# Kernel optimization log

Measured on AMD Instinct MI355X. Metric: run time of the kernel, lower is better.

Reference implementation:

```python
import jax, jax.numpy as jnp
import numpy as np

HIDDEN = 512
HEADS = 8
HEAD_DIM = HIDDEN // HEADS


def setup_inputs() -> dict:
    key = jax.random.key(0)
    ks = jax.random.split(key, 12)
    B, S = 2, 2048
    s = 1.0 / np.sqrt(HIDDEN)
    inp = {
        "query": jax.random.normal(ks[0], (B, S, HIDDEN), dtype=jnp.float32),
        "key": jax.random.normal(ks[1], (B, S, HIDDEN), dtype=jnp.float32),
        "value": jax.random.normal(ks[2], (B, S, HIDDEN), dtype=jnp.float32),
        "Wq": jax.random.uniform(ks[3], (HIDDEN, HIDDEN), jnp.float32, -s, s),
        "bq": jnp.zeros((HIDDEN,), jnp.float32),
        "Wk": jax.random.uniform(ks[4], (HIDDEN, HIDDEN), jnp.float32, -s, s),
        "bk": jnp.zeros((HIDDEN,), jnp.float32),
        "Wv": jax.random.uniform(ks[5], (HIDDEN, HIDDEN), jnp.float32, -s, s),
        "bv": jnp.zeros((HIDDEN,), jnp.float32),
        "Wo": jax.random.uniform(ks[6], (HIDDEN, HIDDEN), jnp.float32, -s, s),
        "bo": jnp.zeros((HIDDEN,), jnp.float32),
    }
    return inp


def reference(query, key, value, Wq, bq, Wk, bk, Wv, bv, Wo, bo):
    B, S, _ = query.shape
    scale = jnp.sqrt(jnp.asarray(HEAD_DIM, dtype=query.dtype))
    # Linear projections (torch Linear: x @ W.T + b)
    Q = (query @ Wq.T + bq).reshape(B, S, HEADS, HEAD_DIM).transpose(0, 2, 1, 3)
    K = (key @ Wk.T + bk).reshape(B, S, HEADS, HEAD_DIM).transpose(0, 2, 1, 3)
    V = (value @ Wv.T + bv).reshape(B, S, HEADS, HEAD_DIM).transpose(0, 2, 1, 3)
    # Scores: [B, H, S, S]
    energy = jnp.einsum("bhqd,bhkd->bhqk", Q, K) / scale
    attn = jax.nn.softmax(energy, axis=-1)
    # Dropout is identity in eval mode.
    x = jnp.einsum("bhqk,bhkd->bhqd", attn, V)
    x = x.transpose(0, 2, 1, 3).reshape(B, S, HIDDEN)
    return x @ Wo.T + bo
```

## Files before the change

### kernel.cpp

```cpp
#include <hip/hip_runtime.h>

typedef __bf16 bf16x8 __attribute__((ext_vector_type(8)));
typedef float f32x4 __attribute__((ext_vector_type(4)));
typedef unsigned int uint4v __attribute__((ext_vector_type(4)));

__device__ __forceinline__ unsigned short f2bf(float f) {
  union { float f; unsigned int u; } v; v.f = f;
  unsigned int u = v.u;
  u += 0x7FFFu + ((u >> 16) & 1u);
  return (unsigned short)(u >> 16);
}

__device__ __forceinline__ unsigned int pack2bf(float a, float b) {
  return (unsigned int)f2bf(a) | ((unsigned int)f2bf(b) << 16);
}

__global__ __launch_bounds__(256) void convert_kernel(
    const float* q, const float* k, const float* v,
    const float* wq, const float* wk, const float* wv, const float* wo,
    unsigned short* qc, unsigned short* kc, unsigned short* vc,
    unsigned short* wqc, unsigned short* wkc, unsigned short* wvc,
    unsigned short* woc, float qscale)
{
  const float* src; unsigned short* dst; int n; float sc = 1.f;
  switch (blockIdx.y) {
    case 0: src = q;  dst = qc;  n = 1 << 21; break;
    case 1: src = k;  dst = kc;  n = 1 << 21; break;
    case 2: src = v;  dst = vc;  n = 1 << 21; break;
    case 3: src = wq; dst = wqc; n = 1 << 18; sc = qscale; break;
    case 4: src = wk; dst = wkc; n = 1 << 18; break;
    case 5: src = wv; dst = wvc; n = 1 << 18; break;
    default: src = wo; dst = woc; n = 1 << 18; break;
  }
  int idx = (blockIdx.x * 256 + threadIdx.x) * 8;
  if (idx >= n) return;
  f32x4 a = *(const f32x4*)(src + idx);
  f32x4 b = *(const f32x4*)(src + idx + 4);
  uint4v p;
  p.x = pack2bf(a.x * sc, a.y * sc);
  p.y = pack2bf(a.z * sc, a.w * sc);
  p.z = pack2bf(b.x * sc, b.y * sc);
  p.w = pack2bf(b.z * sc, b.w * sc);
  *(uint4v*)(dst + idx) = p;
}

template<int OUT>
__device__ __forceinline__ void gemm_core(
    const unsigned short* __restrict__ A, const unsigned short* __restrict__ W,
    const float* __restrict__ bias, void* __restrict__ Cp,
    float bscale, int mbase, int nbase)
{
  __shared__ union {
    struct { unsigned short As[64][40]; unsigned short Bs[128][40]; } t;
    unsigned short Cs[128][72];
  } u;

  const int tid  = threadIdx.x;
  const int wave = tid >> 6, lane = tid & 63;
  const int lrow = lane & 15, lgrp = lane >> 4;

  const int ar = tid >> 2, ac = (tid & 3) * 8;
  const unsigned short* Ag  = A + (size_t)(mbase + ar) * 512 + ac;
  const unsigned short* Bg0 = W + (size_t)(nbase + ar) * 512 + ac;
  const unsigned short* Bg1 = W + (size_t)(nbase + ar + 64) * 512 + ac;

  f32x4 acc[4][2];
#pragma unroll
  for (int i = 0; i < 4; i++)
#pragma unroll
    for (int j = 0; j < 2; j++) acc[i][j] = (f32x4){0.f, 0.f, 0.f, 0.f};

  uint4v pA  = *(const uint4v*)Ag;
  uint4v pB0 = *(const uint4v*)Bg0;
  uint4v pB1 = *(const uint4v*)Bg1;

  for (int kt = 0; kt < 512; kt += 32) {
    __syncthreads();
    *(uint4v*)&u.t.As[ar][ac]      = pA;
    *(uint4v*)&u.t.Bs[ar][ac]      = pB0;
    *(uint4v*)&u.t.Bs[ar + 64][ac] = pB1;
    __syncthreads();
    if (kt + 32 < 512) {
      pA  = *(const uint4v*)(Ag  + kt + 32);
      pB0 = *(const uint4v*)(Bg0 + kt + 32);
      pB1 = *(const uint4v*)(Bg1 + kt + 32);
    }
    bf16x8 a[4], b[2];
#pragma unroll
    for (int mi = 0; mi < 4; mi++)
      a[mi] = *(const bf16x8*)&u.t.As[mi * 16 + lrow][lgrp * 8];
#pragma unroll
    for (int ni = 0; ni < 2; ni++)
      b[ni] = *(const bf16x8*)&u.t.Bs[wave * 32 + ni * 16 + lrow][lgrp * 8];
#pragma unroll
    for (int mi = 0; mi < 4; mi++)
#pragma unroll
      for (int ni = 0; ni < 2; ni++)
        acc[mi][ni] = __builtin_amdgcn_mfma_f32_16x16x32_bf16(
            a[mi], b[ni], acc[mi][ni], 0, 0, 0);
  }

  if constexpr (OUT == 2) {
    __syncthreads();
#pragma unroll
    for (int ni = 0; ni < 2; ni++) {
      int col_l = wave * 32 + ni * 16 + lrow;
      float bv = bias[nbase + col_l];
#pragma unroll
      for (int mi = 0; mi < 4; mi++) {
        int row_l = mi * 16 + lgrp * 4;
#pragma unroll
        for (int r = 0; r < 4; r++)
          u.Cs[col_l][row_l + r] = f2bf(acc[mi][ni][r] + bv);
      }
    }
    __syncthreads();
    const int bb = mbase >> 11, s_base = mbase & 2047;
    unsigned short* Vt = (unsigned short*)Cp;
#pragma unroll
    for (int ks = 0; ks < 4; ks++) {
      int seg = tid + ks * 256;
      int c = seg >> 3, r0 = (seg & 7) * 8;
      uint4v val = *(const uint4v*)&u.Cs[c][r0];
      int n = nbase + c, hh = n >> 6, d = n & 63;
      *(uint4v*)(Vt + ((size_t)(bb * 8 + hh) * 64 + d) * 2048 + s_base + r0) = val;
    }
  } else {
#pragma unroll
    for (int ni = 0; ni < 2; ni++) {
      int col = nbase + wave * 32 + ni * 16 + lrow;
      float bv = bias[col] * bscale;
#pragma unroll
      for (int mi = 0; mi < 4; mi++) {
        int row0 = mbase + mi * 16 + lgrp * 4;
#pragma unroll
        for (int r = 0; r < 4; r++) {
          float val = acc[mi][ni][r] + bv;
          if constexpr (OUT == 0)
            ((unsigned short*)Cp)[(size_t)(row0 + r) * 512 + col] = f2bf(val);
          else
            ((float*)Cp)[(size_t)(row0 + r) * 512 + col] = val;
        }
      }
    }
  }
}

__global__ __launch_bounds__(256) void qkv_gemm(
    const unsigned short* qc, const unsigned short* kc, const unsigned short* vc,
    const unsigned short* wqc, const unsigned short* wkc, const unsigned short* wvc,
    const float* bq, const float* bk, const float* bv,
    unsigned short* Qb, unsigned short* Kb, unsigned short* Vt, float qscale)
{
  const int z = blockIdx.z;
  const int mb = blockIdx.y * 64, nb = blockIdx.x * 128;
  if (z == 2)      gemm_core<2>(vc, wvc, bv, Vt, 1.f, mb, nb);
  else if (z == 0) gemm_core<0>(qc, wqc, bq, Qb, qscale, mb, nb);
  else             gemm_core<0>(kc, wkc, bk, Kb, 1.f, mb, nb);
}

__global__ __launch_bounds__(256) void out_gemm(
    const unsigned short* ctx, const unsigned short* woc,
    const float* bo, float* out)
{
  gemm_core<1>(ctx, woc, bo, out, 1.f, blockIdx.y * 64, blockIdx.x * 128);
}

__global__ __launch_bounds__(256) void attn_kernel(
    const unsigned short* Qb, const unsigned short* Kb,
    const unsigned short* Vt, unsigned short* ctx)
{
  __shared__ unsigned short Ks[128][74];
  __shared__ unsigned short Vs[64][132];
  __shared__ unsigned short Ps[64][132];

  const int tid  = threadIdx.x;
  const int wave = tid >> 6, lane = tid & 63;
  const int lrow = lane & 15, lgrp = lane >> 4;
  const int bh = blockIdx.y, b = bh >> 3, h = bh & 7;
  const int qbase = blockIdx.x * 64;

  const unsigned short* Qg  = Qb + (size_t)(b * 2048 + qbase) * 512 + h * 64;
  const unsigned short* Kg  = Kb + (size_t)(b * 2048) * 512 + h * 64;
  const unsigned short* Vtg = Vt + (size_t)bh * 64 * 2048;

#pragma unroll
  for (int i = 0; i < 2; i++) {
    int seg = tid + i * 256;
    int row = seg >> 3, c0 = (seg & 7) * 8;
    *(uint4v*)&Ps[row][c0] = *(const uint4v*)(Qg + (size_t)row * 512 + c0);
  }
  __syncthreads();
  bf16x8 qf0 = *(const bf16x8*)&Ps[wave * 16 + lrow][lgrp * 8];
  bf16x8 qf1 = *(const bf16x8*)&Ps[wave * 16 + lrow][32 + lgrp * 8];

  const int kr_ = tid >> 3, kc_ = (tid & 7) * 8;
  const int vd_ = tid >> 4, vc_ = (tid & 15) * 8;
  const int slot0 = ((kr_ & 7) << 4) | (kr_ >> 3);

  float lst[4] = {0.f, 0.f, 0.f, 0.f};
  f32x4 oacc[4];
#pragma unroll
  for (int d = 0; d < 4; d++) oacc[d] = (f32x4){0.f, 0.f, 0.f, 0.f};

  uint4v kr[4], vr[4];
#pragma unroll
  for (int i = 0; i < 4; i++) {
    kr[i] = *(const uint4v*)(Kg + (size_t)(kr_ + 32 * i) * 512 + kc_);
    vr[i] = *(const uint4v*)(Vtg + (size_t)(vd_ + 16 * i) * 2048 + vc_);
  }

  for (int it = 0; it < 16; ++it) {
    __syncthreads();
#pragma unroll
    for (int i = 0; i < 4; i++) {
      *(uint4v*)&Ks[slot0 + 4 * i][kc_] = kr[i];
      *(uint4v*)&Vs[vd_ + 16 * i][vc_]  = vr[i];
    }
    __syncthreads();
    if (it < 15) {
      const int key0 = (it + 1) * 128;
#pragma unroll
      for (int i = 0; i < 4; i++) {
        kr[i] = *(const uint4v*)(Kg + (size_t)(key0 + kr_ + 32 * i) * 512 + kc_);
        vr[i] = *(const uint4v*)(Vtg + (size_t)(vd_ + 16 * i) * 2048 + key0 + vc_);
      }
    }

    f32x4 sacc[8];
#pragma unroll
    for (int ni = 0; ni < 8; ni++) sacc[ni] = (f32x4){0.f, 0.f, 0.f, 0.f};
#pragma unroll
    for (int ni = 0; ni < 8; ni++) {
      bf16x8 k0 = *(const bf16x8*)&Ks[ni * 16 + lrow][lgrp * 8];
      bf16x8 k1 = *(const bf16x8*)&Ks[ni * 16 + lrow][32 + lgrp * 8];
      sacc[ni] = __builtin_amdgcn_mfma_f32_16x16x32_bf16(qf0, k0, sacc[ni], 0, 0, 0);
      sacc[ni] = __builtin_amdgcn_mfma_f32_16x16x32_bf16(qf1, k1, sacc[ni], 0, 0, 0);
    }

#pragma unroll
    for (int ni = 0; ni < 8; ni++)
#pragma unroll
      for (int r = 0; r < 4; r++) {
        float p = exp2f(sacc[ni][r]);
        sacc[ni][r] = p;
        lst[r] += p;
      }

#pragma unroll
    for (int r = 0; r < 4; r++) {
      uint4v pk;
      pk.x = pack2bf(sacc[0][r], sacc[1][r]);
      pk.y = pack2bf(sacc[2][r], sacc[3][r]);
      pk.z = pack2bf(sacc[4][r], sacc[5][r]);
      pk.w = pack2bf(sacc[6][r], sacc[7][r]);
      *(uint4v*)&Ps[wave * 16 + lgrp * 4 + r][lrow * 8] = pk;
    }

#pragma unroll
    for (int ks = 0; ks < 4; ks++) {
      bf16x8 pa = *(const bf16x8*)&Ps[wave * 16 + lrow][ks * 32 + lgrp * 8];
#pragma unroll
      for (int dt = 0; dt < 4; dt++) {
        bf16x8 vb = *(const bf16x8*)&Vs[dt * 16 + lrow][ks * 32 + lgrp * 8];
        oacc[dt] = __builtin_amdgcn_mfma_f32_16x16x32_bf16(pa, vb, oacc[dt], 0, 0, 0);
      }
    }
  }

#pragma unroll
  for (int m = 1; m < 16; m <<= 1)
#pragma unroll
    for (int r = 0; r < 4; r++) lst[r] += __shfl_xor(lst[r], m, 64);

  float inv[4];
#pragma unroll
  for (int r = 0; r < 4; r++) inv[r] = 1.0f / lst[r];
  unsigned short* Cg = ctx + (size_t)(b * 2048 + qbase) * 512 + h * 64;
#pragma unroll
  for (int dt = 0; dt < 4; dt++)
#pragma unroll
    for (int r = 0; r < 4; r++) {
      int row = wave * 16 + lgrp * 4 + r;
      int col = dt * 16 + lrow;
      Cg[(size_t)row * 512 + col] = f2bf(oacc[dt][r] * inv[r]);
    }
}

extern "C" void kernel_launch(void* const* d_in, const int* in_sizes, int n_in,
                              void* d_out, int out_size, void* d_ws, size_t ws_size,
                              hipStream_t stream)
{
  const float* q  = (const float*)d_in[0];
  const float* k  = (const float*)d_in[1];
  const float* v  = (const float*)d_in[2];
  const float* Wq = (const float*)d_in[3];
  const float* bq = (const float*)d_in[4];
  const float* Wk = (const float*)d_in[5];
  const float* bk = (const float*)d_in[6];
  const float* Wv = (const float*)d_in[7];
  const float* bv = (const float*)d_in[8];
  const float* Wo = (const float*)d_in[9];
  const float* bo = (const float*)d_in[10];
  float* out = (float*)d_out;

  unsigned short* qc  = (unsigned short*)d_ws;
  unsigned short* kc  = qc  + (size_t)1 * (1 << 21);
  unsigned short* vc  = qc  + (size_t)2 * (1 << 21);
  unsigned short* wqc = qc  + (size_t)3 * (1 << 21);
  unsigned short* wkc = wqc + (1 << 18);
  unsigned short* wvc = wkc + (1 << 18);
  unsigned short* woc = wvc + (1 << 18);
  unsigned short* Qb  = woc + (1 << 18);
  unsigned short* Kb  = Qb  + (1 << 22);
  unsigned short* Vt  = Kb  + (1 << 22);
  unsigned short* Cb  = qc;

  const float qscale = 0.125f * 1.44269504088896340736f;

  convert_kernel<<<dim3(1024, 7), 256, 0, stream>>>(
      q, k, v, Wq, Wk, Wv, Wo, qc, kc, vc, wqc, wkc, wvc, woc, qscale);
  qkv_gemm<<<dim3(4, 64, 3), 256, 0, stream>>>(
      qc, kc, vc, wqc, wkc, wvc, bq, bk, bv, Qb, Kb, Vt, qscale);
  attn_kernel<<<dim3(32, 16), 256, 0, stream>>>(Qb, Kb, Vt, Cb);
  out_gemm<<<dim3(4, 64), 256, 0, stream>>>(Cb, woc, bo, out);
}
```

Before: 165.7 us.

## Fuse activation bf16 conversion into QKV GEMM and double attention query tile

The QKV GEMM now reads fp32 query/key/value directly and packs them to bf16 while staging into shared memory, so the separate conversion pass over the activations is gone. The conversion kernel now handles only the weights. The attention kernel processes 128 queries per block (32 per wave), so each K/V tile loaded into LDS serves twice as many MFMAs. In exchange the grid is halved to 256 blocks and register and LDS use per block rise, which can lower occupancy.

After: 169.8 us. +2.5%, slower.

```diff
diff --git a/kernel.cpp b/kernel.cpp
--- a/kernel.cpp
+++ b/kernel.cpp
@@ -15,25 +15,19 @@
   return (unsigned int)f2bf(a) | ((unsigned int)f2bf(b) << 16);
 }
 
-__global__ __launch_bounds__(256) void convert_kernel(
-    const float* q, const float* k, const float* v,
+__global__ __launch_bounds__(256) void convert_w(
     const float* wq, const float* wk, const float* wv, const float* wo,
-    unsigned short* qc, unsigned short* kc, unsigned short* vc,
     unsigned short* wqc, unsigned short* wkc, unsigned short* wvc,
     unsigned short* woc, float qscale)
 {
-  const float* src; unsigned short* dst; int n; float sc = 1.f;
+  const float* src; unsigned short* dst; float sc = 1.f;
   switch (blockIdx.y) {
-    case 0: src = q;  dst = qc;  n = 1 << 21; break;
-    case 1: src = k;  dst = kc;  n = 1 << 21; break;
-    case 2: src = v;  dst = vc;  n = 1 << 21; break;
-    case 3: src = wq; dst = wqc; n = 1 << 18; sc = qscale; break;
-    case 4: src = wk; dst = wkc; n = 1 << 18; break;
-    case 5: src = wv; dst = wvc; n = 1 << 18; break;
-    default: src = wo; dst = woc; n = 1 << 18; break;
+    case 0: src = wq; dst = wqc; sc = qscale; break;
+    case 1: src = wk; dst = wkc; break;
+    case 2: src = wv; dst = wvc; break;
+    default: src = wo; dst = woc; break;
   }
   int idx = (blockIdx.x * 256 + threadIdx.x) * 8;
-  if (idx >= n) return;
   f32x4 a = *(const f32x4*)(src + idx);
   f32x4 b = *(const f32x4*)(src + idx + 4);
   uint4v p;
@@ -44,9 +38,9 @@
   *(uint4v*)(dst + idx) = p;
 }
 
-template<int OUT>
+template<int OUT, bool AF32>
 __device__ __forceinline__ void gemm_core(
-    const unsigned short* __restrict__ A, const unsigned short* __restrict__ W,
+    const void* __restrict__ Ap, const unsigned short* __restrict__ W,
     const float* __restrict__ bias, void* __restrict__ Cp,
     float bscale, int mbase, int nbase)
 {
@@ -58,9 +52,8 @@
   const int tid  = threadIdx.x;
   const int wave = tid >> 6, lane = tid & 63;
   const int lrow = lane & 15, lgrp = lane >> 4;
-
   const int ar = tid >> 2, ac = (tid & 3) * 8;
-  const unsigned short* Ag  = A + (size_t)(mbase + ar) * 512 + ac;
+
   const unsigned short* Bg0 = W + (size_t)(nbase + ar) * 512 + ac;
   const unsigned short* Bg1 = W + (size_t)(nbase + ar + 64) * 512 + ac;
 
@@ -70,18 +63,40 @@
 #pragma unroll
     for (int j = 0; j < 2; j++) acc[i][j] = (f32x4){0.f, 0.f, 0.f, 0.f};
 
-  uint4v pA  = *(const uint4v*)Ag;
+  const unsigned short* Ab = (const unsigned short*)Ap;
+  const float*          Af = (const float*)Ap;
+  uint4v pA; f32x4 pAf0, pAf1;
+  if constexpr (AF32) {
+    const float* base = Af + (size_t)(mbase + ar) * 512 + ac;
+    pAf0 = *(const f32x4*)(base);
+    pAf1 = *(const f32x4*)(base + 4);
+  } else {
+    pA = *(const uint4v*)(Ab + (size_t)(mbase + ar) * 512 + ac);
+  }
   uint4v pB0 = *(const uint4v*)Bg0;
   uint4v pB1 = *(const uint4v*)Bg1;
 
   for (int kt = 0; kt < 512; kt += 32) {
     __syncthreads();
-    *(uint4v*)&u.t.As[ar][ac]      = pA;
+    if constexpr (AF32) {
+      uint4v w;
+      w.x = pack2bf(pAf0.x, pAf0.y); w.y = pack2bf(pAf0.z, pAf0.w);
+      w.z = pack2bf(pAf1.x, pAf1.y); w.w = pack2bf(pAf1.z, pAf1.w);
+      *(uint4v*)&u.t.As[ar][ac] = w;
+    } else {
+      *(uint4v*)&u.t.As[ar][ac] = pA;
+    }
     *(uint4v*)&u.t.Bs[ar][ac]      = pB0;
     *(uint4v*)&u.t.Bs[ar + 64][ac] = pB1;
     __syncthreads();
     if (kt + 32 < 512) {
-      pA  = *(const uint4v*)(Ag  + kt + 32);
+      if constexpr (AF32) {
+        const float* base = Af + (size_t)(mbase + ar) * 512 + ac + kt + 32;
+        pAf0 = *(const f32x4*)(base);
+        pAf1 = *(const f32x4*)(base + 4);
+      } else {
+        pA = *(const uint4v*)(Ab + (size_t)(mbase + ar) * 512 + ac + kt + 32);
+      }
       pB0 = *(const uint4v*)(Bg0 + kt + 32);
       pB1 = *(const uint4v*)(Bg1 + kt + 32);
     }
@@ -147,23 +162,24 @@
 }
 
 __global__ __launch_bounds__(256) void qkv_gemm(
-    const unsigned short* qc, const unsigned short* kc, const unsigned short* vc,
-    const unsigned short* wqc, const unsigned short* wkc, const unsigned short* wvc,
+    const float* q, const float* k, const float* v,
+    const unsigned short* wqc, const unsigned short* wkc,
+    const unsigned short* wvc,
     const float* bq, const float* bk, const float* bv,
     unsigned short* Qb, unsigned short* Kb, unsigned short* Vt, float qscale)
 {
   const int z = blockIdx.z;
   const int mb = blockIdx.y * 64, nb = blockIdx.x * 128;
-  if (z == 2)      gemm_core<2>(vc, wvc, bv, Vt, 1.f, mb, nb);
-  else if (z == 0) gemm_core<0>(qc, wqc, bq, Qb, qscale, mb, nb);
-  else             gemm_core<0>(kc, wkc, bk, Kb, 1.f, mb, nb);
+  if (z == 2)      gemm_core<2, true>(v, wvc, bv, Vt, 1.f, mb, nb);
+  else if (z == 0) gemm_core<0, true>(q, wqc, bq, Qb, qscale, mb, nb);
+  else             gemm_core<0, true>(k, wkc, bk, Kb, 1.f, mb, nb);
 }
 
 __global__ __launch_bounds__(256) void out_gemm(
     const unsigned short* ctx, const unsigned short* woc,
     const float* bo, float* out)
 {
-  gemm_core<1>(ctx, woc, bo, out, 1.f, blockIdx.y * 64, blockIdx.x * 128);
+  gemm_core<1, false>(ctx, woc, bo, out, 1.f, blockIdx.y * 64, blockIdx.x * 128);
 }
 
 __global__ __launch_bounds__(256) void attn_kernel(
@@ -171,42 +187,48 @@
     const unsigned short* Vt, unsigned short* ctx)
 {
   __shared__ unsigned short Ks[128][74];
-  __shared__ unsigned short Vs[64][132];
-  __shared__ unsigned short Ps[64][132];
+  __shared__ unsigned short Vs[64][134];
+  __shared__ unsigned short Ps[128][134];
 
   const int tid  = threadIdx.x;
   const int wave = tid >> 6, lane = tid & 63;
   const int lrow = lane & 15, lgrp = lane >> 4;
   const int bh = blockIdx.y, b = bh >> 3, h = bh & 7;
-  const int qbase = blockIdx.x * 64;
+  const int qbase = blockIdx.x * 128;
 
   const unsigned short* Qg  = Qb + (size_t)(b * 2048 + qbase) * 512 + h * 64;
   const unsigned short* Kg  = Kb + (size_t)(b * 2048) * 512 + h * 64;
   const unsigned short* Vtg = Vt + (size_t)bh * 64 * 2048;
 
 #pragma unroll
-  for (int i = 0; i < 2; i++) {
+  for (int i = 0; i < 4; i++) {
     int seg = tid + i * 256;
     int row = seg >> 3, c0 = (seg & 7) * 8;
     *(uint4v*)&Ps[row][c0] = *(const uint4v*)(Qg + (size_t)row * 512 + c0);
   }
   __syncthreads();
-  bf16x8 qf0 = *(const bf16x8*)&Ps[wave * 16 + lrow][lgrp * 8];
-  bf16x8 qf1 = *(const bf16x8*)&Ps[wave * 16 + lrow][32 + lgrp * 8];
-
-  const int kr_ = tid >> 3, kc_ = (tid & 7) * 8;
+  bf16x8 qf[2][2];
+#pragma unroll
+  for (int mi = 0; mi < 2; mi++)
+#pragma unroll
+    for (int kh = 0; kh < 2; kh++)
+      qf[mi][kh] = *(const bf16x8*)&Ps[wave * 32 + mi * 16 + lrow][kh * 32 + lgrp * 8];
+
+  const int s0  = tid >> 3, kc_ = (tid & 7) * 8;
+  const int krow0 = ((s0 & 15) << 3) | (s0 >> 4);
   const int vd_ = tid >> 4, vc_ = (tid & 15) * 8;
-  const int slot0 = ((kr_ & 7) << 4) | (kr_ >> 3);
-
-  float lst[4] = {0.f, 0.f, 0.f, 0.f};
-  f32x4 oacc[4];
-#pragma unroll
-  for (int d = 0; d < 4; d++) oacc[d] = (f32x4){0.f, 0.f, 0.f, 0.f};
+
+  float lst[2][4] = {{0.f,0.f,0.f,0.f},{0.f,0.f,0.f,0.f}};
+  f32x4 oacc[2][4];
+#pragma unroll
+  for (int mi = 0; mi < 2; mi++)
+#pragma unroll
+    for (int d = 0; d < 4; d++) oacc[mi][d] = (f32x4){0.f, 0.f, 0.f, 0.f};
 
   uint4v kr[4], vr[4];
 #pragma unroll
   for (int i = 0; i < 4; i++) {
-    kr[i] = *(const uint4v*)(Kg + (size_t)(kr_ + 32 * i) * 512 + kc_);
+    kr[i] = *(const uint4v*)(Kg + (size_t)(krow0 + 2 * i) * 512 + kc_);
     vr[i] = *(const uint4v*)(Vtg + (size_t)(vd_ + 16 * i) * 2048 + vc_);
   }
 
@@ -214,56 +236,70 @@
     __syncthreads();
 #pragma unroll
     for (int i = 0; i < 4; i++) {
-      *(uint4v*)&Ks[slot0 + 4 * i][kc_] = kr[i];
-      *(uint4v*)&Vs[vd_ + 16 * i][vc_]  = vr[i];
+      *(uint4v*)&Ks[s0 + 32 * i][kc_]  = kr[i];
+      *(uint4v*)&Vs[vd_ + 16 * i][vc_] = vr[i];
     }
     __syncthreads();
     if (it < 15) {
       const int key0 = (it + 1) * 128;
 #pragma unroll
       for (int i = 0; i < 4; i++) {
-        kr[i] = *(const uint4v*)(Kg + (size_t)(key0 + kr_ + 32 * i) * 512 + kc_);
+        kr[i] = *(const uint4v*)(Kg + (size_t)(key0 + krow0 + 2 * i) * 512 + kc_);
         vr[i] = *(const uint4v*)(Vtg + (size_t)(vd_ + 16 * i) * 2048 + key0 + vc_);
       }
     }
 
-    f32x4 sacc[8];
-#pragma unroll
-    for (int ni = 0; ni < 8; ni++) sacc[ni] = (f32x4){0.f, 0.f, 0.f, 0.f};
+    f32x4 sacc[2][8];
+#pragma unroll
+    for (int mi = 0; mi < 2; mi++)
+#pragma unroll
+      for (int ni = 0; ni < 8; ni++) sacc[mi][ni] = (f32x4){0.f, 0.f, 0.f, 0.f};
 #pragma unroll
     for (int ni = 0; ni < 8; ni++) {
       bf16x8 k0 = *(const bf16x8*)&Ks[ni * 16 + lrow][lgrp * 8];
       bf16x8 k1 = *(const bf16x8*)&Ks[ni * 16 + lrow][32 + lgrp * 8];
-      sacc[ni] = __builtin_amdgcn_mfma_f32_16x16x32_bf16(qf0, k0, sacc[ni], 0, 0, 0);
-      sacc[ni] = __builtin_amdgcn_mfma_f32_16x16x32_bf16(qf1, k1, sacc[ni], 0, 0, 0);
-    }
-
-#pragma unroll
-    for (int ni = 0; ni < 8; ni++)
+#pragma unroll
+      for (int mi = 0; mi < 2; mi++) {
+        sacc[mi][ni] = __builtin_amdgcn_mfma_f32_16x16x32_bf16(qf[mi][0], k0, sacc[mi][ni], 0, 0, 0);
+        sacc[mi][ni] = __builtin_amdgcn_mfma_f32_16x16x32_bf16(qf[mi][1], k1, sacc[mi][ni], 0, 0, 0);
+      }
+    }
+
+#pragma unroll
+    for (int mi = 0; mi < 2; mi++)
+#pragma unroll
+      for (int ni = 0; ni < 8; ni++)
+#pragma unroll
+        for (int r = 0; r < 4; r++) {
+          float p = exp2f(sacc[mi][ni][r]);
+          sacc[mi][ni][r] = p;
+          lst[mi][r] += p;
+        }
+
+#pragma unroll
+    for (int mi = 0; mi < 2; mi++)
 #pragma unroll
       for (int r = 0; r < 4; r++) {
-        float p = exp2f(sacc[ni][r]);
-        sacc[ni][r] = p;
-        lst[r] += p;
-      }
-
-#pragma unroll
-    for (int r = 0; r < 4; r++) {
-      uint4v pk;
-      pk.x = pack2bf(sacc[0][r], sacc[1][r]);
-      pk.y = pack2bf(sacc[2][r], sacc[3][r]);
-      pk.z = pack2bf(sacc[4][r], sacc[5][r]);
-      pk.w = pack2bf(sacc[6][r], sacc[7][r]);
-      *(uint4v*)&Ps[wave * 16 + lgrp * 4 + r][lrow * 8] = pk;
-    }
+        uint4v pk;
+        pk.x = pack2bf(sacc[mi][0][r], sacc[mi][1][r]);
+        pk.y = pack2bf(sacc[mi][2][r], sacc[mi][3][r]);
+        pk.z = pack2bf(sacc[mi][4][r], sacc[mi][5][r]);
+        pk.w = pack2bf(sacc[mi][6][r], sacc[mi][7][r]);
+        *(uint4v*)&Ps[wave * 32 + mi * 16 + lgrp * 4 + r][lrow * 8] = pk;
+      }
 
 #pragma unroll
     for (int ks = 0; ks < 4; ks++) {
-      bf16x8 pa = *(const bf16x8*)&Ps[wave * 16 + lrow][ks * 32 + lgrp * 8];
+      bf16x8 pa[2];
+#pragma unroll
+      for (int mi = 0; mi < 2; mi++)
+        pa[mi] = *(const bf16x8*)&Ps[wave * 32 + mi * 16 + lrow][ks * 32 + lgrp * 8];
 #pragma unroll
       for (int dt = 0; dt < 4; dt++) {
         bf16x8 vb = *(const bf16x8*)&Vs[dt * 16 + lrow][ks * 32 + lgrp * 8];
-        oacc[dt] = __builtin_amdgcn_mfma_f32_16x16x32_bf16(pa, vb, oacc[dt], 0, 0, 0);
+#pragma unroll
+        for (int mi = 0; mi < 2; mi++)
+          oacc[mi][dt] = __builtin_amdgcn_mfma_f32_16x16x32_bf16(pa[mi], vb, oacc[mi][dt], 0, 0, 0);
       }
     }
   }
@@ -271,20 +307,25 @@
 #pragma unroll
   for (int m = 1; m < 16; m <<= 1)
 #pragma unroll
-    for (int r = 0; r < 4; r++) lst[r] += __shfl_xor(lst[r], m, 64);
-
-  float inv[4];
-#pragma unroll
-  for (int r = 0; r < 4; r++) inv[r] = 1.0f / lst[r];
+    for (int mi = 0; mi < 2; mi++)
+#pragma unroll
+      for (int r = 0; r < 4; r++) lst[mi][r] += __shfl_xor(lst[mi][r], m, 64);
+
   unsigned short* Cg = ctx + (size_t)(b * 2048 + qbase) * 512 + h * 64;
 #pragma unroll
-  for (int dt = 0; dt < 4; dt++)
-#pragma unroll
-    for (int r = 0; r < 4; r++) {
-      int row = wave * 16 + lgrp * 4 + r;
-      int col = dt * 16 + lrow;
-      Cg[(size_t)row * 512 + col] = f2bf(oacc[dt][r] * inv[r]);
-    }
+  for (int mi = 0; mi < 2; mi++) {
+    float inv[4];
+#pragma unroll
+    for (int r = 0; r < 4; r++) inv[r] = 1.0f / lst[mi][r];
+#pragma unroll
+    for (int dt = 0; dt < 4; dt++)
+#pragma unroll
+      for (int r = 0; r < 4; r++) {
+        int row = wave * 32 + mi * 16 + lgrp * 4 + r;
+        int col = dt * 16 + lrow;
+        Cg[(size_t)row * 512 + col] = f2bf(oacc[mi][dt][r] * inv[r]);
+      }
+  }
 }
 
 extern "C" void kernel_launch(void* const* d_in, const int* in_sizes, int n_in,
@@ -304,24 +345,21 @@
   const float* bo = (const float*)d_in[10];
   float* out = (float*)d_out;
 
-  unsigned short* qc  = (unsigned short*)d_ws;
-  unsigned short* kc  = qc  + (size_t)1 * (1 << 21);
-  unsigned short* vc  = qc  + (size_t)2 * (1 << 21);
-  unsigned short* wqc = qc  + (size_t)3 * (1 << 21);
+  unsigned short* wqc = (unsigned short*)d_ws;
   unsigned short* wkc = wqc + (1 << 18);
   unsigned short* wvc = wkc + (1 << 18);
   unsigned short* woc = wvc + (1 << 18);
   unsigned short* Qb  = woc + (1 << 18);
-  unsigned short* Kb  = Qb  + (1 << 22);
-  unsigned short* Vt  = Kb  + (1 << 22);
-  unsigned short* Cb  = qc;
+  unsigned short* Kb  = Qb  + (1 << 21);
+  unsigned short* Vt  = Kb  + (1 << 21);
+  unsigned short* Cb  = Vt  + (1 << 21);
 
   const float qscale = 0.125f * 1.44269504088896340736f;
 
-  convert_kernel<<<dim3(1024, 7), 256, 0, stream>>>(
-      q, k, v, Wq, Wk, Wv, Wo, qc, kc, vc, wqc, wkc, wvc, woc, qscale);
+  convert_w<<<dim3(128, 4), 256, 0, stream>>>(
+      Wq, Wk, Wv, Wo, wqc, wkc, wvc, woc, qscale);
   qkv_gemm<<<dim3(4, 64, 3), 256, 0, stream>>>(
-      qc, kc, vc, wqc, wkc, wvc, bq, bk, bv, Qb, Kb, Vt, qscale);
-  attn_kernel<<<dim3(32, 16), 256, 0, stream>>>(Qb, Kb, Vt, Cb);
+      q, k, v, wqc, wkc, wvc, bq, bk, bv, Qb, Kb, Vt, qscale);
+  attn_kernel<<<dim3(16, 16), 256, 0, stream>>>(Qb, Kb, Vt, Cb);
   out_gemm<<<dim3(4, 64), 256, 0, stream>>>(Cb, woc, bo, out);
 }
```
